# Performance work log

Measured on AMD Instinct MI355X. Metric: run time of the kernel, lower is better.

## Reference

```python
import jax, jax.numpy as jnp
import numpy as np

B, S, H = 4, 2048, 2048      # batch, seq, hidden_size
E, K, F = 8, 2, 1408         # n_routed_experts, topk, moe_inter_dim


def setup_inputs() -> dict:
    key = jax.random.key(0)
    k0, k1, k2, k3, k4 = jax.random.split(key, 5)
    s = 0.02  # init scale for weights
    return {
        "hidden_states": jax.random.normal(k0, (B, S, H), dtype=jnp.float32),
        "router_w": jax.random.normal(k1, (E, H), dtype=jnp.float32) * s,
        "gate_w": jax.random.normal(k2, (E, F, H), dtype=jnp.float32) * s,
        "up_w": jax.random.normal(k3, (E, F, H), dtype=jnp.float32) * s,
        "down_w": jax.random.normal(k4, (E, H, F), dtype=jnp.float32) * s,
    }


def reference(hidden_states, router_w, gate_w, up_w, down_w):
    shape = hidden_states.shape
    x = hidden_states.reshape(-1, H)                  # [T, H], T = B*S
    # Router: softmax over all experts, then top-k of the probabilities
    logits = x @ router_w.T                            # [T, E]
    weights = jax.nn.softmax(logits, axis=-1)          # [T, E]
    topk_weight, indices = jax.lax.top_k(weights, K)   # [T, K]
    # normalize_top_k_affinities
    topk_weight = topk_weight / (topk_weight.sum(axis=-1, keepdims=True) + 1e-20)
    # Per-token per-expert combine weight: [T, E]
    combine = jnp.einsum("tk,tke->te", topk_weight,
                         jax.nn.one_hot(indices, E, dtype=topk_weight.dtype))
    # Experts: swiglu MLP, weighted-combined. Loop over the small fixed set of experts.
    out = jnp.zeros_like(x)
    for e in range(E):
        h = jax.nn.silu(x @ gate_w[e].T) * (x @ up_w[e].T)  # [T, F]
        out = out + combine[:, e:e + 1] * (h @ down_w[e].T)  # [T, H]
    return out.reshape(shape)
```

## Files before the change

kernel.cpp:

```cpp
#include <hip/hip_runtime.h>
#include <stdint.h>

#define T_TOK 8192
#define HD 2048
#define NE 8
#define FD 1408
#define BM 128
#define BN 128
#define BK 64
#define MAXT 136
#define ROWS_CAP 17408

typedef unsigned short u16;
typedef __attribute__((ext_vector_type(8))) short bf16x8;
typedef __attribute__((ext_vector_type(4))) float f32x4;

__device__ __forceinline__ u16 f2bf(float f) {
  unsigned u = __float_as_uint(f);
  unsigned r = (u + 0x7fffu + ((u >> 16) & 1u)) >> 16;
  return (u16)r;
}
__device__ __forceinline__ float bflo(unsigned u) { return __uint_as_float(u << 16); }
__device__ __forceinline__ float bfhi(unsigned u) { return __uint_as_float(u & 0xffff0000u); }

__device__ __forceinline__ void async_copy16(const void* g, void* l) {
  __builtin_amdgcn_global_load_lds(
      (__attribute__((address_space(1))) void*)(uintptr_t)g,
      (__attribute__((address_space(3))) void*)(uintptr_t)l,
      16, 0, 0);
}

__device__ __forceinline__ void conv4(const float* __restrict__ s, u16* __restrict__ d, long j) {
  float4 v = ((const float4*)s)[j];
  ushort4 o;
  o.x = f2bf(v.x); o.y = f2bf(v.y); o.z = f2bf(v.z); o.w = f2bf(v.w);
  ((ushort4*)d)[j] = o;
}

__global__ __launch_bounds__(256) void k_router(
    const float* __restrict__ x, const float* __restrict__ rw,
    const float* __restrict__ gw, const float* __restrict__ uw, const float* __restrict__ dw,
    u16* __restrict__ xb, u16* __restrict__ gwb, u16* __restrict__ uwb, u16* __restrict__ dwb,
    int* __restrict__ topk_idx, float* __restrict__ topk_w)
{
  int t = blockIdx.x;
  int tid = threadIdx.x;
  int lane = tid & 63;
  int wave = tid >> 6;
  const float4* xr = (const float4*)(x + (size_t)t * HD);
  const float4* w0 = (const float4*)(rw + (size_t)(wave * 2) * HD);
  const float4* w1 = (const float4*)(rw + (size_t)(wave * 2 + 1) * HD);
  float a0 = 0.f, a1 = 0.f;
  for (int i = lane; i < HD / 4; i += 64) {
    float4 xv = xr[i], v0 = w0[i], v1 = w1[i];
    a0 += xv.x * v0.x + xv.y * v0.y + xv.z * v0.z + xv.w * v0.w;
    a1 += xv.x * v1.x + xv.y * v1.y + xv.z * v1.z + xv.w * v1.w;
  }
  {
    float4 v0 = xr[tid * 2], v1 = xr[tid * 2 + 1];
    uint4 o;
    o.x = (unsigned)f2bf(v0.x) | ((unsigned)f2bf(v0.y) << 16);
    o.y = (unsigned)f2bf(v0.z) | ((unsigned)f2bf(v0.w) << 16);
    o.z = (unsigned)f2bf(v1.x) | ((unsigned)f2bf(v1.y) << 16);
    o.w = (unsigned)f2bf(v1.z) | ((unsigned)f2bf(v1.w) << 16);
    ((uint4*)(xb + (size_t)t * HD))[tid] = o;
  }
#pragma unroll
  for (int off = 32; off > 0; off >>= 1) {
    a0 += __shfl_down(a0, off);
    a1 += __shfl_down(a1, off);
  }
  __shared__ float lg[NE];
  if (lane == 0) { lg[wave * 2] = a0; lg[wave * 2 + 1] = a1; }
  __syncthreads();
  if (tid == 0) {
    float m1 = lg[0], m2 = -3.4e38f;
    int i1 = 0, i2 = 0;
    for (int e = 1; e < NE; e++) {
      float v = lg[e];
      if (v > m1)      { m2 = m1; i2 = i1; m1 = v; i1 = e; }
      else if (v > m2) { m2 = v; i2 = e; }
    }
    float wA = 1.f / (1.f + expf(m2 - m1));
    float wB = 1.f - wA;
    topk_idx[t * 2] = i1; topk_idx[t * 2 + 1] = i2;
    topk_w[t * 2] = wA;   topk_w[t * 2 + 1] = wB;
  }
  const long n_w = (long)NE * FD * HD / 4;
  const long gstride = (long)gridDim.x * 256;
  const long g0 = (long)t * 256 + tid;
  for (long j = g0; j < n_w; j += gstride) conv4(gw, gwb, j);
  for (long j = g0; j < n_w; j += gstride) conv4(uw, uwb, j);
  for (long j = g0; j < n_w; j += gstride) conv4(dw, dwb, j);
}

__global__ __launch_bounds__(256) void k_meta_scatter(
    const int* __restrict__ topk_idx, int* __restrict__ meta,
    int* __restrict__ row_token, int* __restrict__ tokrow)
{
  __shared__ int scan[NE][257];
  __shared__ int roff[NE], tstart[NE + 1];
  int tid = threadIdx.x;
  for (int i = tid; i < ROWS_CAP; i += 256) row_token[i] = 0;
  if (tid < NE) scan[tid][0] = 0;
  int cnt[NE] = {};
  int base_i = tid * 64;
#pragma unroll 4
  for (int j = 0; j < 64; j++) {
    int v = topk_idx[base_i + j];
#pragma unroll
    for (int e = 0; e < NE; e++) cnt[e] += (v == e);
  }
  int i = tid + 1;
#pragma unroll
  for (int e = 0; e < NE; e++) scan[e][i] = cnt[e];
  __syncthreads();
  for (int s = 1; s < 256; s <<= 1) {
    int add[NE];
#pragma unroll
    for (int e = 0; e < NE; e++) add[e] = (i >= s) ? scan[e][i - s] : 0;
    __syncthreads();
#pragma unroll
    for (int e = 0; e < NE; e++) scan[e][i] += add[e];
    __syncthreads();
  }
  if (tid == 0) {
    int off = 0, nt = 0;
    for (int e = 0; e < NE; e++) {
      int tot = scan[e][256];
      int tiles = (tot + BM - 1) / BM;
      roff[e] = off;
      tstart[e] = nt;
      nt += tiles;
      off += tiles * BM;
    }
    tstart[NE] = nt;
    meta[8] = nt;
  }
  __syncthreads();
  int nt = tstart[NE];
  if (tid < nt) {
    int e = 0;
#pragma unroll
    for (int k = 1; k < NE; k++) e += (tid >= tstart[k]);
    meta[64 + tid] = e;
    meta[256 + tid] = roff[e] + (tid - tstart[e]) * BM;
  }
  int pos[NE];
#pragma unroll
  for (int e = 0; e < NE; e++) pos[e] = roff[e] + scan[e][tid];
  for (int j = 0; j < 64; j++) {
    int idx = base_i + j;
    int v = topk_idx[idx];
    int p = 0;
#pragma unroll
    for (int e = 0; e < NE; e++) if (v == e) p = pos[e]++;
    row_token[p] = idx >> 1;
    tokrow[idx] = p;
  }
}

__global__ __launch_bounds__(256, 2) void k_gemm1(
    const u16* __restrict__ xb, const u16* __restrict__ gwb, const u16* __restrict__ uwb,
    const int* __restrict__ meta, const int* __restrict__ row_token, u16* __restrict__ hb)
{
  int total = meta[8];
  int tile = blockIdx.x;
  if (tile >= total) return;
  int e = meta[64 + tile];
  int row0 = meta[256 + tile];
  int ntile = blockIdx.y;

  __shared__ u16 As[BM * BK];
  __shared__ u16 Bg[BN * BK];
  __shared__ u16 Bu[BN * BK];

  int lane = threadIdx.x & 63;
  int wave = threadIdx.x >> 6;
  int wr = wave >> 1, wc = wave & 1;

  const u16* aG[4]; const u16* gG[4]; const u16* uG[4];
  unsigned ldsOff[4];
#pragma unroll
  for (int j = 0; j < 4; j++) {
    int r = wave * 32 + j * 8 + (lane >> 3);
    int c = (lane & 7) ^ (r & 7);
    int tok = row_token[row0 + r];
    aG[j] = xb + (size_t)tok * HD + c * 8;
    int nrow = ntile * BN + r;
    size_t wof = ((size_t)e * FD + nrow) * HD + c * 8;
    gG[j] = gwb + wof;
    uG[j] = uwb + wof;
    ldsOff[j] = (unsigned)(wave * 32 + j * 8) * 128;
  }

  f32x4 accG[4][4] = {};
  f32x4 accU[4][4] = {};

  for (int kt = 0; kt < HD / BK; kt++) {
    int ko = kt * BK;
#pragma unroll
    for (int j = 0; j < 4; j++) async_copy16(aG[j] + ko, (char*)As + ldsOff[j]);
#pragma unroll
    for (int j = 0; j < 4; j++) async_copy16(gG[j] + ko, (char*)Bg + ldsOff[j]);
#pragma unroll
    for (int j = 0; j < 4; j++) async_copy16(uG[j] + ko, (char*)Bu + ldsOff[j]);
    __syncthreads();
#pragma unroll
    for (int kk = 0; kk < 2; kk++) {
      bf16x8 av[4], gv[4], uv[4];
#pragma unroll
      for (int mi = 0; mi < 4; mi++) {
        int r = wr * 64 + mi * 16 + (lane & 15);
        int slot = (kk * 4 + (lane >> 4)) ^ (r & 7);
        av[mi] = *(const bf16x8*)((const char*)As + (unsigned)(r * 8 + slot) * 16);
      }
#pragma unroll
      for (int ni = 0; ni < 4; ni++) {
        int r = wc * 64 + ni * 16 + (lane & 15);
        int slot = (kk * 4 + (lane >> 4)) ^ (r & 7);
        gv[ni] = *(const bf16x8*)((const char*)Bg + (unsigned)(r * 8 + slot) * 16);
        uv[ni] = *(const bf16x8*)((const char*)Bu + (unsigned)(r * 8 + slot) * 16);
      }
#pragma unroll
      for (int mi = 0; mi < 4; mi++)
#pragma unroll
        for (int ni = 0; ni < 4; ni++) {
          accG[mi][ni] = __builtin_amdgcn_mfma_f32_16x16x32_bf16(av[mi], gv[ni], accG[mi][ni], 0, 0, 0);
          accU[mi][ni] = __builtin_amdgcn_mfma_f32_16x16x32_bf16(av[mi], uv[ni], accU[mi][ni], 0, 0, 0);
        }
    }
    __syncthreads();
  }

#pragma unroll
  for (int mi = 0; mi < 4; mi++) {
#pragma unroll
    for (int r = 0; r < 4; r++) {
      int row = row0 + wr * 64 + mi * 16 + (lane >> 4) * 4 + r;
      u16* hrow = hb + (size_t)row * FD + ntile * BN + wc * 64 + (lane & 15);
#pragma unroll
      for (int ni = 0; ni < 4; ni++) {
        float g = accG[mi][ni][r];
        float u = accU[mi][ni][r];
        float s = g / (1.f + __expf(-g));
        hrow[ni * 16] = f2bf(s * u);
      }
    }
  }
}

__global__ __launch_bounds__(256, 3) void k_gemm2(
    const u16* __restrict__ hb, const u16* __restrict__ dwb,
    const int* __restrict__ meta, u16* __restrict__ Y)
{
  int total = meta[8];
  int tile = blockIdx.x;
  if (tile >= total) return;
  int e = meta[64 + tile];
  int row0 = meta[256 + tile];
  int ntile = blockIdx.y;

  __shared__ u16 As[BM * BK];
  __shared__ u16 Bs[BN * BK];

  int lane = threadIdx.x & 63;
  int wave = threadIdx.x >> 6;
  int wr = wave >> 1, wc = wave & 1;

  const u16* aG[4]; const u16* bG[4];
  unsigned ldsOff[4];
#pragma unroll
  for (int j = 0; j < 4; j++) {
    int r = wave * 32 + j * 8 + (lane >> 3);
    int c = (lane & 7) ^ (r & 7);
    aG[j] = hb + (size_t)(row0 + r) * FD + c * 8;
    int nrow = ntile * BN + r;
    bG[j] = dwb + ((size_t)e * HD + nrow) * FD + c * 8;
    ldsOff[j] = (unsigned)(wave * 32 + j * 8) * 128;
  }

  f32x4 acc[4][4] = {};

  for (int kt = 0; kt < FD / BK; kt++) {
    int ko = kt * BK;
#pragma unroll
    for (int j = 0; j < 4; j++) async_copy16(aG[j] + ko, (char*)As + ldsOff[j]);
#pragma unroll
    for (int j = 0; j < 4; j++) async_copy16(bG[j] + ko, (char*)Bs + ldsOff[j]);
    __syncthreads();
#pragma unroll
    for (int kk = 0; kk < 2; kk++) {
      bf16x8 av[4], bv[4];
#pragma unroll
      for (int mi = 0; mi < 4; mi++) {
        int r = wr * 64 + mi * 16 + (lane & 15);
        int slot = (kk * 4 + (lane >> 4)) ^ (r & 7);
        av[mi] = *(const bf16x8*)((const char*)As + (unsigned)(r * 8 + slot) * 16);
      }
#pragma unroll
      for (int ni = 0; ni < 4; ni++) {
        int r = wc * 64 + ni * 16 + (lane & 15);
        int slot = (kk * 4 + (lane >> 4)) ^ (r & 7);
        bv[ni] = *(const bf16x8*)((const char*)Bs + (unsigned)(r * 8 + slot) * 16);
      }
#pragma unroll
      for (int mi = 0; mi < 4; mi++)
#pragma unroll
        for (int ni = 0; ni < 4; ni++)
          acc[mi][ni] = __builtin_amdgcn_mfma_f32_16x16x32_bf16(av[mi], bv[ni], acc[mi][ni], 0, 0, 0);
    }
    __syncthreads();
  }

#pragma unroll
  for (int mi = 0; mi < 4; mi++) {
#pragma unroll
    for (int r = 0; r < 4; r++) {
      int grow = row0 + wr * 64 + mi * 16 + (lane >> 4) * 4 + r;
      u16* yrow = Y + (size_t)grow * HD + ntile * BN + wc * 64 + (lane & 15);
#pragma unroll
      for (int ni = 0; ni < 4; ni++)
        yrow[ni * 16] = f2bf(acc[mi][ni][r]);
    }
  }
}

__global__ __launch_bounds__(256) void k_combine(
    const u16* __restrict__ Y, const int* __restrict__ tokrow,
    const float* __restrict__ topk_w, float* __restrict__ out)
{
  int t = blockIdx.x;
  int i = threadIdx.x;
  int rA = tokrow[t * 2], rB = tokrow[t * 2 + 1];
  float wA = topk_w[t * 2], wB = topk_w[t * 2 + 1];
  uint4 a = *(const uint4*)(Y + (size_t)rA * HD + i * 8);
  uint4 b = *(const uint4*)(Y + (size_t)rB * HD + i * 8);
  float4 o0, o1;
  o0.x = wA * bflo(a.x) + wB * bflo(b.x);
  o0.y = wA * bfhi(a.x) + wB * bfhi(b.x);
  o0.z = wA * bflo(a.y) + wB * bflo(b.y);
  o0.w = wA * bfhi(a.y) + wB * bfhi(b.y);
  o1.x = wA * bflo(a.z) + wB * bflo(b.z);
  o1.y = wA * bfhi(a.z) + wB * bfhi(b.z);
  o1.z = wA * bflo(a.w) + wB * bflo(b.w);
  o1.w = wA * bfhi(a.w) + wB * bfhi(b.w);
  float* op = out + (size_t)t * HD + i * 8;
  *(float4*)op = o0;
  *(float4*)(op + 4) = o1;
}

extern "C" void kernel_launch(void* const* d_in, const int* in_sizes, int n_in,
                              void* d_out, int out_size, void* d_ws, size_t ws_size,
                              hipStream_t stream) {
  const float* x  = (const float*)d_in[0];
  const float* rw = (const float*)d_in[1];
  const float* gw = (const float*)d_in[2];
  const float* uw = (const float*)d_in[3];
  const float* dw = (const float*)d_in[4];
  float* out = (float*)d_out;

  char* w = (char*)d_ws;
  int*   meta      = (int*)w;
  int*   row_token = (int*)(w + 4096);
  int*   topk_idx  = (int*)(w + 4096 + ROWS_CAP * 4);
  float* topk_w    = (float*)(w + 4096 + ROWS_CAP * 4 + T_TOK * 2 * 4);
  int*   tokrow    = (int*)(w + 4096 + ROWS_CAP * 4 + T_TOK * 4 * 4);
  size_t off = (size_t)1 << 20;
  u16* xb  = (u16*)(w + off); off += (size_t)T_TOK * HD * 2;
  u16* gwb = (u16*)(w + off); off += (size_t)NE * FD * HD * 2;
  u16* uwb = (u16*)(w + off); off += (size_t)NE * FD * HD * 2;
  u16* dwb = (u16*)(w + off); off += (size_t)NE * HD * FD * 2;
  u16* hb  = (u16*)(w + off);
  u16* Y = xb;

  k_router<<<T_TOK, 256, 0, stream>>>(x, rw, gw, uw, dw, xb, gwb, uwb, dwb, topk_idx, topk_w);
  k_meta_scatter<<<1, 256, 0, stream>>>(topk_idx, meta, row_token, tokrow);
  k_gemm1<<<dim3(MAXT, FD / BN), 256, 0, stream>>>(xb, gwb, uwb, meta, row_token, hb);
  k_gemm2<<<dim3(MAXT, HD / BN), 256, 0, stream>>>(hb, dwb, meta, Y);
  k_combine<<<T_TOK, 256, 0, stream>>>(Y, tokrow, topk_w, out);
}
```

Before: 726.9 us.

## Double-buffer LDS in expert GEMMs with larger 256-row tiles and 512-thread blocks

Both grouped GEMM kernels now use 512-thread blocks with 256-row M tiles (and 256-wide N tiles for the down projection), BK reduced to 32, and double-buffered LDS so the next K slice's async loads overlap the current MFMAs. The block index is remapped so that consecutive blocks spread across experts, and s_setprio wraps the MFMA section. The aim is to hide global-load latency and raise weight reuse per tile. In exchange, padding per expert grows with the larger tiles, the LDS layout drops the XOR swizzle (bank conflicts are possible), and there are more barriers per unit of K. The meta/scatter routine must produce 256-row tiles for this to be correct, which depends on the BM macro in hidden code.

```diff
diff --git a/kernel.cpp b/kernel.cpp
--- a/kernel.cpp
+++ b/kernel.cpp
@@ -5,11 +5,10 @@
 #define HD 2048
 #define NE 8
 #define FD 1408
-#define BM 128
-#define BN 128
-#define BK 64
-#define MAXT 136
-#define ROWS_CAP 17408
+#define BM 256
+#define BK 32
+#define MAXT 72
+#define ROWS_CAP 18432
 
 typedef unsigned short u16;
 typedef __attribute__((ext_vector_type(8))) short bf16x8;
@@ -160,77 +159,83 @@
   }
 }
 
-__global__ __launch_bounds__(256, 2) void k_gemm1(
+__global__ __launch_bounds__(512, 2) void k_gemm1(
     const u16* __restrict__ xb, const u16* __restrict__ gwb, const u16* __restrict__ uwb,
     const int* __restrict__ meta, const int* __restrict__ row_token, u16* __restrict__ hb)
 {
   int total = meta[8];
-  int tile = blockIdx.x;
-  if (tile >= total) return;
-  int e = meta[64 + tile];
-  int row0 = meta[256 + tile];
+  int mt = (int)blockIdx.x;
+  mt = (mt & 7) * 9 + (mt >> 3);
+  if (mt >= total) return;
+  int e = meta[64 + mt];
+  int row0 = meta[256 + mt];
   int ntile = blockIdx.y;
 
-  __shared__ u16 As[BM * BK];
-  __shared__ u16 Bg[BN * BK];
-  __shared__ u16 Bu[BN * BK];
-
-  int lane = threadIdx.x & 63;
-  int wave = threadIdx.x >> 6;
+  __shared__ u16 As[2][BM * BK];
+  __shared__ u16 Bgs[2][128 * BK];
+  __shared__ u16 Bus[2][128 * BK];
+
+  int tid = threadIdx.x;
+  int lane = tid & 63;
+  int wave = tid >> 6;
   int wr = wave >> 1, wc = wave & 1;
 
-  const u16* aG[4]; const u16* gG[4]; const u16* uG[4];
-  unsigned ldsOff[4];
-#pragma unroll
-  for (int j = 0; j < 4; j++) {
-    int r = wave * 32 + j * 8 + (lane >> 3);
-    int c = (lane & 7) ^ (r & 7);
-    int tok = row_token[row0 + r];
-    aG[j] = xb + (size_t)tok * HD + c * 8;
-    int nrow = ntile * BN + r;
-    size_t wof = ((size_t)e * FD + nrow) * HD + c * 8;
-    gG[j] = gwb + wof;
-    uG[j] = uwb + wof;
-    ldsOff[j] = (unsigned)(wave * 32 + j * 8) * 128;
-  }
+  int rowA = tid & 255;
+  int tok = row_token[row0 + rowA];
+  const u16* aSrc0 = xb + (size_t)tok * HD + ((0 * 2 + (tid >> 8)) * 8);
+  const u16* aSrc1 = xb + (size_t)tok * HD + ((1 * 2 + (tid >> 8)) * 8);
+  int rowB = tid & 127;
+  int slotB = tid >> 7;
+  size_t wof = ((size_t)e * FD + (size_t)ntile * 128 + rowB) * HD + slotB * 8;
+  const u16* gSrc = gwb + wof;
+  const u16* uSrc = uwb + wof;
+  const unsigned ldsA0 = (unsigned)((0 * 512 + wave * 64) * 16);
+  const unsigned ldsA1 = (unsigned)((1 * 512 + wave * 64) * 16);
+  const unsigned ldsB  = (unsigned)((wave * 64) * 16);
+
+  const unsigned aRd = (unsigned)((lane >> 4) * 256 + wr * 64 + (lane & 15));
+  const unsigned bRd = (unsigned)((lane >> 4) * 128 + wc * 64 + (lane & 15));
 
   f32x4 accG[4][4] = {};
   f32x4 accU[4][4] = {};
 
+  {
+    async_copy16(aSrc0, (char*)As[0] + ldsA0);
+    async_copy16(aSrc1, (char*)As[0] + ldsA1);
+    async_copy16(gSrc, (char*)Bgs[0] + ldsB);
+    async_copy16(uSrc, (char*)Bus[0] + ldsB);
+  }
+  __syncthreads();
+
+  int cur = 0;
   for (int kt = 0; kt < HD / BK; kt++) {
-    int ko = kt * BK;
-#pragma unroll
-    for (int j = 0; j < 4; j++) async_copy16(aG[j] + ko, (char*)As + ldsOff[j]);
-#pragma unroll
-    for (int j = 0; j < 4; j++) async_copy16(gG[j] + ko, (char*)Bg + ldsOff[j]);
-#pragma unroll
-    for (int j = 0; j < 4; j++) async_copy16(uG[j] + ko, (char*)Bu + ldsOff[j]);
+    if (kt + 1 < HD / BK) {
+      int ko = (kt + 1) * BK;
+      async_copy16(aSrc0 + ko, (char*)As[cur ^ 1] + ldsA0);
+      async_copy16(aSrc1 + ko, (char*)As[cur ^ 1] + ldsA1);
+      async_copy16(gSrc + ko, (char*)Bgs[cur ^ 1] + ldsB);
+      async_copy16(uSrc + ko, (char*)Bus[cur ^ 1] + ldsB);
+    }
+    bf16x8 av[4], gv[4], uv[4];
+#pragma unroll
+    for (int mi = 0; mi < 4; mi++)
+      av[mi] = *(const bf16x8*)((const char*)As[cur] + (aRd + mi * 16) * 16);
+#pragma unroll
+    for (int ni = 0; ni < 4; ni++) {
+      gv[ni] = *(const bf16x8*)((const char*)Bgs[cur] + (bRd + ni * 16) * 16);
+      uv[ni] = *(const bf16x8*)((const char*)Bus[cur] + (bRd + ni * 16) * 16);
+    }
+    __builtin_amdgcn_s_setprio(1);
+#pragma unroll
+    for (int mi = 0; mi < 4; mi++)
+#pragma unroll
+      for (int ni = 0; ni < 4; ni++) {
+        accG[mi][ni] = __builtin_amdgcn_mfma_f32_16x16x32_bf16(av[mi], gv[ni], accG[mi][ni], 0, 0, 0);
+        accU[mi][ni] = __builtin_amdgcn_mfma_f32_16x16x32_bf16(av[mi], uv[ni], accU[mi][ni], 0, 0, 0);
+      }
+    __builtin_amdgcn_s_setprio(0);
     __syncthreads();
-#pragma unroll
-    for (int kk = 0; kk < 2; kk++) {
-      bf16x8 av[4], gv[4], uv[4];
-#pragma unroll
-      for (int mi = 0; mi < 4; mi++) {
-        int r = wr * 64 + mi * 16 + (lane & 15);
-        int slot = (kk * 4 + (lane >> 4)) ^ (r & 7);
-        av[mi] = *(const bf16x8*)((const char*)As + (unsigned)(r * 8 + slot) * 16);
-      }
-#pragma unroll
-      for (int ni = 0; ni < 4; ni++) {
-        int r = wc * 64 + ni * 16 + (lane & 15);
-        int slot = (kk * 4 + (lane >> 4)) ^ (r & 7);
-        gv[ni] = *(const bf16x8*)((const char*)Bg + (unsigned)(r * 8 + slot) * 16);
-        uv[ni] = *(const bf16x8*)((const char*)Bu + (unsigned)(r * 8 + slot) * 16);
-      }
-#pragma unroll
-      for (int mi = 0; mi < 4; mi++)
-#pragma unroll
-        for (int ni = 0; ni < 4; ni++) {
-          accG[mi][ni] = __builtin_amdgcn_mfma_f32_16x16x32_bf16(av[mi], gv[ni], accG[mi][ni], 0, 0, 0);
-          accU[mi][ni] = __builtin_amdgcn_mfma_f32_16x16x32_bf16(av[mi], uv[ni], accU[mi][ni], 0, 0, 0);
-        }
-    }
-    __syncthreads();
+    cur ^= 1;
   }
 
 #pragma unroll
@@ -238,7 +243,7 @@
 #pragma unroll
     for (int r = 0; r < 4; r++) {
       int row = row0 + wr * 64 + mi * 16 + (lane >> 4) * 4 + r;
-      u16* hrow = hb + (size_t)row * FD + ntile * BN + wc * 64 + (lane & 15);
+      u16* hrow = hb + (size_t)row * FD + (size_t)ntile * 128 + wc * 64 + (lane & 15);
 #pragma unroll
       for (int ni = 0; ni < 4; ni++) {
         float g = accG[mi][ni][r];
@@ -250,75 +255,81 @@
   }
 }
 
-__global__ __launch_bounds__(256, 3) void k_gemm2(
+__global__ __launch_bounds__(512, 2) void k_gemm2(
     const u16* __restrict__ hb, const u16* __restrict__ dwb,
     const int* __restrict__ meta, u16* __restrict__ Y)
 {
   int total = meta[8];
-  int tile = blockIdx.x;
-  if (tile >= total) return;
-  int e = meta[64 + tile];
-  int row0 = meta[256 + tile];
+  int mt = (int)blockIdx.x;
+  mt = (mt & 7) * 9 + (mt >> 3);
+  if (mt >= total) return;
+  int e = meta[64 + mt];
+  int row0 = meta[256 + mt];
   int ntile = blockIdx.y;
 
-  __shared__ u16 As[BM * BK];
-  __shared__ u16 Bs[BN * BK];
-
-  int lane = threadIdx.x & 63;
-  int wave = threadIdx.x >> 6;
-  int wr = wave >> 1, wc = wave & 1;
-
-  const u16* aG[4]; const u16* bG[4];
-  unsigned ldsOff[4];
-#pragma unroll
-  for (int j = 0; j < 4; j++) {
-    int r = wave * 32 + j * 8 + (lane >> 3);
-    int c = (lane & 7) ^ (r & 7);
-    aG[j] = hb + (size_t)(row0 + r) * FD + c * 8;
-    int nrow = ntile * BN + r;
-    bG[j] = dwb + ((size_t)e * HD + nrow) * FD + c * 8;
-    ldsOff[j] = (unsigned)(wave * 32 + j * 8) * 128;
-  }
-
-  f32x4 acc[4][4] = {};
-
+  __shared__ u16 As[2][BM * BK];
+  __shared__ u16 Bs[2][256 * BK];
+
+  int tid = threadIdx.x;
+  int lane = tid & 63;
+  int wave = tid >> 6;
+  int wr = wave >> 2, wc = wave & 3;
+
+  int rowA = tid & 255;
+  const u16* aSrc0 = hb + (size_t)(row0 + rowA) * FD + ((0 * 2 + (tid >> 8)) * 8);
+  const u16* aSrc1 = hb + (size_t)(row0 + rowA) * FD + ((1 * 2 + (tid >> 8)) * 8);
+  size_t bof = ((size_t)e * HD + (size_t)ntile * 256 + rowA) * FD;
+  const u16* bSrc0 = dwb + bof + ((0 * 2 + (tid >> 8)) * 8);
+  const u16* bSrc1 = dwb + bof + ((1 * 2 + (tid >> 8)) * 8);
+  const unsigned lds0 = (unsigned)((0 * 512 + wave * 64) * 16);
+  const unsigned lds1 = (unsigned)((1 * 512 + wave * 64) * 16);
+
+  const unsigned aRd = (unsigned)((lane >> 4) * 256 + wr * 128 + (lane & 15));
+  const unsigned bRd = (unsigned)((lane >> 4) * 256 + wc * 64 + (lane & 15));
+
+  f32x4 acc[8][4] = {};
+
+  {
+    async_copy16(aSrc0, (char*)As[0] + lds0);
+    async_copy16(aSrc1, (char*)As[0] + lds1);
+    async_copy16(bSrc0, (char*)Bs[0] + lds0);
+    async_copy16(bSrc1, (char*)Bs[0] + lds1);
+  }
+  __syncthreads();
+
+  int cur = 0;
   for (int kt = 0; kt < FD / BK; kt++) {
-    int ko = kt * BK;
-#pragma unroll
-    for (int j = 0; j < 4; j++) async_copy16(aG[j] + ko, (char*)As + ldsOff[j]);
-#pragma unroll
-    for (int j = 0; j < 4; j++) async_copy16(bG[j] + ko, (char*)Bs + ldsOff[j]);
+    if (kt + 1 < FD / BK) {
+      int ko = (kt + 1) * BK;
+      async_copy16(aSrc0 + ko, (char*)As[cur ^ 1] + lds0);
+      async_copy16(aSrc1 + ko, (char*)As[cur ^ 1] + lds1);
+      async_copy16(bSrc0 + ko, (char*)Bs[cur ^ 1] + lds0);
+      async_copy16(bSrc1 + ko, (char*)Bs[cur ^ 1] + lds1);
+    }
+    bf16x8 av[8], bv[4];
+#pragma unroll
+    for (int mi = 0; mi < 8; mi++)
+      av[mi] = *(const bf16x8*)((const char*)As[cur] + (aRd + mi * 16) * 16);
+#pragma unroll
+    for (int ni = 0; ni < 4; ni++)
+      bv[ni] = *(const bf16x8*)((const char*)Bs[cur] + (bRd + ni * 16) * 16);
+    __builtin_amdgcn_s_setprio(1);
+#pragma unroll
+    for (int mi = 0; mi < 8; mi++)
+#pragma unroll
+      for (int ni = 0; ni < 4; ni++)
+        acc[mi][ni] = __builtin_amdgcn_mfma_f32_16x16x32_bf16(av[mi], bv[ni], acc[mi][ni], 0, 0, 0);
+    __builtin_amdgcn_s_setprio(0);
     __syncthreads();
-#pragma unroll
-    for (int kk = 0; kk < 2; kk++) {
-      bf16x8 av[4], bv[4];
-#pragma unroll
-      for (int mi = 0; mi < 4; mi++) {
-        int r = wr * 64 + mi * 16 + (lane & 15);
-        int slot = (kk * 4 + (lane >> 4)) ^ (r & 7);
-        av[mi] = *(const bf16x8*)((const char*)As + (unsigned)(r * 8 + slot) * 16);
-      }
-#pragma unroll
-      for (int ni = 0; ni < 4; ni++) {
-        int r = wc * 64 + ni * 16 + (lane & 15);
-        int slot = (kk * 4 + (lane >> 4)) ^ (r & 7);
-        bv[ni] = *(const bf16x8*)((const char*)Bs + (unsigned)(r * 8 + slot) * 16);
-      }
-#pragma unroll
-      for (int mi = 0; mi < 4; mi++)
-#pragma unroll
-        for (int ni = 0; ni < 4; ni++)
-          acc[mi][ni] = __builtin_amdgcn_mfma_f32_16x16x32_bf16(av[mi], bv[ni], acc[mi][ni], 0, 0, 0);
-    }
-    __syncthreads();
-  }
-
-#pragma unroll
-  for (int mi = 0; mi < 4; mi++) {
+    cur ^= 1;
+  }
+
+#pragma unroll
+  for (int mi = 0; mi < 8; mi++) {
 #pragma unroll
     for (int r = 0; r < 4; r++) {
-      int grow = row0 + wr * 64 + mi * 16 + (lane >> 4) * 4 + r;
-      u16* yrow = Y + (size_t)grow * HD + ntile * BN + wc * 64 + (lane & 15);
+      int grow = row0 + wr * 128 + mi * 16 + (lane >> 4) * 4 + r;
+      u16* yrow = Y + (size_t)grow * HD + (size_t)ntile * 256 + wc * 64 + (lane & 15);
 #pragma unroll
       for (int ni = 0; ni < 4; ni++)
         yrow[ni * 16] = f2bf(acc[mi][ni][r]);
@@ -376,7 +387,7 @@
 
   k_router<<<T_TOK, 256, 0, stream>>>(x, rw, gw, uw, dw, xb, gwb, uwb, dwb, topk_idx, topk_w);
   k_meta_scatter<<<1, 256, 0, stream>>>(topk_idx, meta, row_token, tokrow);
-  k_gemm1<<<dim3(MAXT, FD / BN), 256, 0, stream>>>(xb, gwb, uwb, meta, row_token, hb);
-  k_gemm2<<<dim3(MAXT, HD / BN), 256, 0, stream>>>(hb, dwb, meta, Y);
+  k_gemm1<<<dim3(MAXT, FD / 128), 512, 0, stream>>>(xb, gwb, uwb, meta, row_token, hb);
+  k_gemm2<<<dim3(MAXT, HD / 256), 512, 0, stream>>>(hb, dwb, meta, Y);
   k_combine<<<T_TOK, 256, 0, stream>>>(Y, tokrow, topk_w, out);
 }
```

New measurement: 1.040 ms. 43.1% more time.

## Double-buffer LDS in expert GEMMs, enlarge M tile to 256 with 512 threads

Applied to the files above, without the earlier changes.

Both grouped GEMMs now use double-buffered shared memory, so the next K slice is prefetched asynchronously while MFMAs run on the current one, and each iteration needs one barrier instead of two. The M tile grows to 256 rows with 8 waves per block, which halves the number of M tiles and reuses each weight tile across more tokens. Tile indices are remapped so that blocks with adjacent blockIdx interleave across experts, and s_setprio raises wave priority around the MFMA bursts. In exchange, LDS use per block roughly quadruples, which may lower occupancy, and padding waste per expert grows with the larger tile.

```diff
diff --git a/kernel.cpp b/kernel.cpp
--- a/kernel.cpp
+++ b/kernel.cpp
@@ -5,11 +5,12 @@
 #define HD 2048
 #define NE 8
 #define FD 1408
-#define BM 128
-#define BN 128
+#define BM 256
+#define BN1 128
+#define BN2 128
 #define BK 64
-#define MAXT 136
-#define ROWS_CAP 17408
+#define MAXT 72
+#define ROWS_CAP 18432
 
 typedef unsigned short u16;
 typedef __attribute__((ext_vector_type(8))) short bf16x8;
@@ -160,52 +161,71 @@
   }
 }
 
-__global__ __launch_bounds__(256, 2) void k_gemm1(
+__global__ __launch_bounds__(512, 2) void k_gemm1(
     const u16* __restrict__ xb, const u16* __restrict__ gwb, const u16* __restrict__ uwb,
     const int* __restrict__ meta, const int* __restrict__ row_token, u16* __restrict__ hb)
 {
   int total = meta[8];
-  int tile = blockIdx.x;
-  if (tile >= total) return;
-  int e = meta[64 + tile];
-  int row0 = meta[256 + tile];
+  int mt = (int)blockIdx.x;
+  mt = (mt & 7) * 9 + (mt >> 3);
+  if (mt >= total) return;
+  int e = meta[64 + mt];
+  int row0 = meta[256 + mt];
   int ntile = blockIdx.y;
 
-  __shared__ u16 As[BM * BK];
-  __shared__ u16 Bg[BN * BK];
-  __shared__ u16 Bu[BN * BK];
+  __shared__ u16 As[2][BM * BK];
+  __shared__ u16 Bg[2][BN1 * BK];
+  __shared__ u16 Bu[2][BN1 * BK];
 
   int lane = threadIdx.x & 63;
   int wave = threadIdx.x >> 6;
   int wr = wave >> 1, wc = wave & 1;
 
-  const u16* aG[4]; const u16* gG[4]; const u16* uG[4];
-  unsigned ldsOff[4];
+  const u16* aG[4]; unsigned aOff[4];
+  const u16* gG[2]; const u16* uG[2]; unsigned bOff[2];
 #pragma unroll
   for (int j = 0; j < 4; j++) {
     int r = wave * 32 + j * 8 + (lane >> 3);
     int c = (lane & 7) ^ (r & 7);
     int tok = row_token[row0 + r];
     aG[j] = xb + (size_t)tok * HD + c * 8;
-    int nrow = ntile * BN + r;
+    aOff[j] = (unsigned)(wave * 32 + j * 8) * 128;
+  }
+#pragma unroll
+  for (int j = 0; j < 2; j++) {
+    int r = wave * 16 + j * 8 + (lane >> 3);
+    int c = (lane & 7) ^ (r & 7);
+    int nrow = ntile * BN1 + r;
     size_t wof = ((size_t)e * FD + nrow) * HD + c * 8;
     gG[j] = gwb + wof;
     uG[j] = uwb + wof;
-    ldsOff[j] = (unsigned)(wave * 32 + j * 8) * 128;
+    bOff[j] = (unsigned)(wave * 16 + j * 8) * 128;
   }
 
   f32x4 accG[4][4] = {};
   f32x4 accU[4][4] = {};
 
+#pragma unroll
+  for (int j = 0; j < 4; j++) async_copy16(aG[j], (char*)As[0] + aOff[j]);
+#pragma unroll
+  for (int j = 0; j < 2; j++) async_copy16(gG[j], (char*)Bg[0] + bOff[j]);
+#pragma unroll
+  for (int j = 0; j < 2; j++) async_copy16(uG[j], (char*)Bu[0] + bOff[j]);
+  asm volatile("s_waitcnt vmcnt(0)" ::: "memory");
+  __builtin_amdgcn_sched_barrier(0);
+  __builtin_amdgcn_s_barrier();
+
+  int cur = 0;
   for (int kt = 0; kt < HD / BK; kt++) {
-    int ko = kt * BK;
-#pragma unroll
-    for (int j = 0; j < 4; j++) async_copy16(aG[j] + ko, (char*)As + ldsOff[j]);
-#pragma unroll
-    for (int j = 0; j < 4; j++) async_copy16(gG[j] + ko, (char*)Bg + ldsOff[j]);
-#pragma unroll
-    for (int j = 0; j < 4; j++) async_copy16(uG[j] + ko, (char*)Bu + ldsOff[j]);
-    __syncthreads();
+    if (kt + 1 < HD / BK) {
+      int ko = (kt + 1) * BK;
+#pragma unroll
+      for (int j = 0; j < 4; j++) async_copy16(aG[j] + ko, (char*)As[cur ^ 1] + aOff[j]);
+#pragma unroll
+      for (int j = 0; j < 2; j++) async_copy16(gG[j] + ko, (char*)Bg[cur ^ 1] + bOff[j]);
+#pragma unroll
+      for (int j = 0; j < 2; j++) async_copy16(uG[j] + ko, (char*)Bu[cur ^ 1] + bOff[j]);
+    }
 #pragma unroll
     for (int kk = 0; kk < 2; kk++) {
       bf16x8 av[4], gv[4], uv[4];
@@ -213,15 +233,16 @@
       for (int mi = 0; mi < 4; mi++) {
         int r = wr * 64 + mi * 16 + (lane & 15);
         int slot = (kk * 4 + (lane >> 4)) ^ (r & 7);
-        av[mi] = *(const bf16x8*)((const char*)As + (unsigned)(r * 8 + slot) * 16);
+        av[mi] = *(const bf16x8*)((const char*)As[cur] + (unsigned)(r * 8 + slot) * 16);
       }
 #pragma unroll
       for (int ni = 0; ni < 4; ni++) {
         int r = wc * 64 + ni * 16 + (lane & 15);
         int slot = (kk * 4 + (lane >> 4)) ^ (r & 7);
-        gv[ni] = *(const bf16x8*)((const char*)Bg + (unsigned)(r * 8 + slot) * 16);
-        uv[ni] = *(const bf16x8*)((const char*)Bu + (unsigned)(r * 8 + slot) * 16);
+        gv[ni] = *(const bf16x8*)((const char*)Bg[cur] + (unsigned)(r * 8 + slot) * 16);
+        uv[ni] = *(const bf16x8*)((const char*)Bu[cur] + (unsigned)(r * 8 + slot) * 16);
       }
+      __builtin_amdgcn_s_setprio(1);
 #pragma unroll
       for (int mi = 0; mi < 4; mi++)
 #pragma unroll
@@ -229,8 +250,12 @@
           accG[mi][ni] = __builtin_amdgcn_mfma_f32_16x16x32_bf16(av[mi], gv[ni], accG[mi][ni], 0, 0, 0);
           accU[mi][ni] = __builtin_amdgcn_mfma_f32_16x16x32_bf16(av[mi], uv[ni], accU[mi][ni], 0, 0, 0);
         }
-    }
-    __syncthreads();
+      __builtin_amdgcn_s_setprio(0);
+    }
+    asm volatile("s_waitcnt vmcnt(0)" ::: "memory");
+    __builtin_amdgcn_sched_barrier(0);
+    __builtin_amdgcn_s_barrier();
+    cur ^= 1;
   }
 
 #pragma unroll
@@ -238,7 +263,7 @@
 #pragma unroll
     for (int r = 0; r < 4; r++) {
       int row = row0 + wr * 64 + mi * 16 + (lane >> 4) * 4 + r;
-      u16* hrow = hb + (size_t)row * FD + ntile * BN + wc * 64 + (lane & 15);
+      u16* hrow = hb + (size_t)row * FD + ntile * BN1 + wc * 64 + (lane & 15);
 #pragma unroll
       for (int ni = 0; ni < 4; ni++) {
         float g = accG[mi][ni][r];
@@ -250,45 +275,62 @@
   }
 }
 
-__global__ __launch_bounds__(256, 3) void k_gemm2(
+__global__ __launch_bounds__(512, 2) void k_gemm2(
     const u16* __restrict__ hb, const u16* __restrict__ dwb,
     const int* __restrict__ meta, u16* __restrict__ Y)
 {
   int total = meta[8];
-  int tile = blockIdx.x;
-  if (tile >= total) return;
-  int e = meta[64 + tile];
-  int row0 = meta[256 + tile];
+  int mt = (int)blockIdx.x;
+  mt = (mt & 7) * 9 + (mt >> 3);
+  if (mt >= total) return;
+  int e = meta[64 + mt];
+  int row0 = meta[256 + mt];
   int ntile = blockIdx.y;
 
-  __shared__ u16 As[BM * BK];
-  __shared__ u16 Bs[BN * BK];
+  __shared__ u16 As[2][BM * BK];
+  __shared__ u16 Bs[2][BN2 * BK];
 
   int lane = threadIdx.x & 63;
   int wave = threadIdx.x >> 6;
   int wr = wave >> 1, wc = wave & 1;
 
-  const u16* aG[4]; const u16* bG[4];
-  unsigned ldsOff[4];
+  const u16* aG[4]; unsigned aOff[4];
+  const u16* bG[2]; unsigned bOff[2];
 #pragma unroll
   for (int j = 0; j < 4; j++) {
     int r = wave * 32 + j * 8 + (lane >> 3);
     int c = (lane & 7) ^ (r & 7);
     aG[j] = hb + (size_t)(row0 + r) * FD + c * 8;
-    int nrow = ntile * BN + r;
+    aOff[j] = (unsigned)(wave * 32 + j * 8) * 128;
+  }
+#pragma unroll
+  for (int j = 0; j < 2; j++) {
+    int r = wave * 16 + j * 8 + (lane >> 3);
+    int c = (lane & 7) ^ (r & 7);
+    int nrow = ntile * BN2 + r;
     bG[j] = dwb + ((size_t)e * HD + nrow) * FD + c * 8;
-    ldsOff[j] = (unsigned)(wave * 32 + j * 8) * 128;
+    bOff[j] = (unsigned)(wave * 16 + j * 8) * 128;
   }
 
   f32x4 acc[4][4] = {};
 
+#pragma unroll
+  for (int j = 0; j < 4; j++) async_copy16(aG[j], (char*)As[0] + aOff[j]);
+#pragma unroll
+  for (int j = 0; j < 2; j++) async_copy16(bG[j], (char*)Bs[0] + bOff[j]);
+  asm volatile("s_waitcnt vmcnt(0)" ::: "memory");
+  __builtin_amdgcn_sched_barrier(0);
+  __builtin_amdgcn_s_barrier();
+
+  int cur = 0;
   for (int kt = 0; kt < FD / BK; kt++) {
-    int ko = kt * BK;
-#pragma unroll
-    for (int j = 0; j < 4; j++) async_copy16(aG[j] + ko, (char*)As + ldsOff[j]);
-#pragma unroll
-    for (int j = 0; j < 4; j++) async_copy16(bG[j] + ko, (char*)Bs + ldsOff[j]);
-    __syncthreads();
+    if (kt + 1 < FD / BK) {
+      int ko = (kt + 1) * BK;
+#pragma unroll
+      for (int j = 0; j < 4; j++) async_copy16(aG[j] + ko, (char*)As[cur ^ 1] + aOff[j]);
+#pragma unroll
+      for (int j = 0; j < 2; j++) async_copy16(bG[j] + ko, (char*)Bs[cur ^ 1] + bOff[j]);
+    }
 #pragma unroll
     for (int kk = 0; kk < 2; kk++) {
       bf16x8 av[4], bv[4];
@@ -296,21 +338,26 @@
       for (int mi = 0; mi < 4; mi++) {
         int r = wr * 64 + mi * 16 + (lane & 15);
         int slot = (kk * 4 + (lane >> 4)) ^ (r & 7);
-        av[mi] = *(const bf16x8*)((const char*)As + (unsigned)(r * 8 + slot) * 16);
+        av[mi] = *(const bf16x8*)((const char*)As[cur] + (unsigned)(r * 8 + slot) * 16);
       }
 #pragma unroll
       for (int ni = 0; ni < 4; ni++) {
         int r = wc * 64 + ni * 16 + (lane & 15);
         int slot = (kk * 4 + (lane >> 4)) ^ (r & 7);
-        bv[ni] = *(const bf16x8*)((const char*)Bs + (unsigned)(r * 8 + slot) * 16);
+        bv[ni] = *(const bf16x8*)((const char*)Bs[cur] + (unsigned)(r * 8 + slot) * 16);
       }
+      __builtin_amdgcn_s_setprio(1);
 #pragma unroll
       for (int mi = 0; mi < 4; mi++)
 #pragma unroll
         for (int ni = 0; ni < 4; ni++)
           acc[mi][ni] = __builtin_amdgcn_mfma_f32_16x16x32_bf16(av[mi], bv[ni], acc[mi][ni], 0, 0, 0);
-    }
-    __syncthreads();
+      __builtin_amdgcn_s_setprio(0);
+    }
+    asm volatile("s_waitcnt vmcnt(0)" ::: "memory");
+    __builtin_amdgcn_sched_barrier(0);
+    __builtin_amdgcn_s_barrier();
+    cur ^= 1;
   }
 
 #pragma unroll
@@ -318,7 +365,7 @@
 #pragma unroll
     for (int r = 0; r < 4; r++) {
       int grow = row0 + wr * 64 + mi * 16 + (lane >> 4) * 4 + r;
-      u16* yrow = Y + (size_t)grow * HD + ntile * BN + wc * 64 + (lane & 15);
+      u16* yrow = Y + (size_t)grow * HD + ntile * BN2 + wc * 64 + (lane & 15);
 #pragma unroll
       for (int ni = 0; ni < 4; ni++)
         yrow[ni * 16] = f2bf(acc[mi][ni][r]);
@@ -376,7 +423,7 @@
 
   k_router<<<T_TOK, 256, 0, stream>>>(x, rw, gw, uw, dw, xb, gwb, uwb, dwb, topk_idx, topk_w);
   k_meta_scatter<<<1, 256, 0, stream>>>(topk_idx, meta, row_token, tokrow);
-  k_gemm1<<<dim3(MAXT, FD / BN), 256, 0, stream>>>(xb, gwb, uwb, meta, row_token, hb);
-  k_gemm2<<<dim3(MAXT, HD / BN), 256, 0, stream>>>(hb, dwb, meta, Y);
+  k_gemm1<<<dim3(MAXT, FD / BN1), 512, 0, stream>>>(xb, gwb, uwb, meta, row_token, hb);
+  k_gemm2<<<dim3(MAXT, HD / BN2), 512, 0, stream>>>(hb, dwb, meta, Y);
   k_combine<<<T_TOK, 256, 0, stream>>>(Y, tokrow, topk_w, out);
 }
```

Result: slower. 747.7 us (+2.9%).
